# Optimization experiments

Measured on AMD Instinct MI355X. Metric: run time of the kernel, lower is better.

## Reference

```python
import jax, jax.numpy as jnp
import numpy as np

T, H, I, E, TOP_K = 4096, 2048, 1024, 16, 2
I_SHARED = 1024  # moe_intermediate_size * n_shared_experts


def _silu_and_mul(gu):
    g, u = jnp.split(gu, 2, axis=-1)
    return jax.nn.silu(g) * u


def setup_inputs() -> dict:
    key = jax.random.key(0)
    ks = jax.random.split(key, 8)
    s = 0.02
    return {
        "hidden_states": jax.random.normal(ks[0], (T, H), jnp.float32),
        "gate_w": jax.random.normal(ks[1], (E, H), jnp.float32) * s,          # router
        "w1": jax.random.normal(ks[2], (E, 2 * I, H), jnp.float32) * s,       # expert gate_up
        "b1": jax.random.normal(ks[3], (E, 2 * I), jnp.float32) * s,
        "w2": jax.random.normal(ks[4], (E, H, I), jnp.float32) * s,           # expert down
        "sg_w": jax.random.normal(ks[5], (2 * I_SHARED, H), jnp.float32) * s, # shared gate_up
        "sg_b": jax.random.normal(ks[6], (2 * I_SHARED,), jnp.float32) * s,
        "sd_w": jax.random.normal(ks[7], (H, I_SHARED), jnp.float32) * s,     # shared down
    }


def reference(hidden_states, gate_w, w1, b1, w2, sg_w, sg_b, sd_w):
    x = hidden_states  # [T, H]

    # shared expert MLP (gate_up has bias, down does not)
    shared = _silu_and_mul(x @ sg_w.T + sg_b) @ sd_w.T  # [T, H]

    # router: softmax -> top-k -> renormalize (norm_topk_prob=True)
    probs = jax.nn.softmax(x @ gate_w.T, axis=-1)       # [T, E]
    wts, idx = jax.lax.top_k(probs, TOP_K)              # [T, k]
    wts = wts / jnp.sum(wts, axis=-1, keepdims=True)

    # per-expert combine coefficient: coef[e, t] = sum_k wts[t,k] * (idx[t,k]==e)
    coef = jnp.sum(jax.nn.one_hot(idx, E, dtype=x.dtype) * wts[..., None], axis=1).T  # [E, T]

    def body(acc, params):
        w1e, b1e, w2e, ce = params
        a = _silu_and_mul(x @ w1e.T + b1e)   # [T, I]
        return acc + ce[:, None] * (a @ w2e.T), None

    out, _ = jax.lax.scan(body, jnp.zeros_like(x), (w1, b1, w2, coef))
    return out + shared
```

## Files before the change

kernel.cpp:

```cpp
#include <hip/hip_runtime.h>
#include <hip/hip_bf16.h>
#include <stdint.h>

#define T_TOK 4096
#define H_DIM 2048
#define I_DIM 1024
#define NEXP  16
#define NROWS 16384

typedef short bf16x8 __attribute__((ext_vector_type(8)));
typedef float f32x4  __attribute__((ext_vector_type(4)));
typedef unsigned short u16;
typedef unsigned short u16x8 __attribute__((ext_vector_type(8)));

__device__ __forceinline__ u16 f2b(float f) {
  union { __hip_bfloat16 h; u16 u; } cv;
  cv.h = __float2bfloat16(f);
  return cv.u;
}

__device__ __forceinline__ void gload16(const void* g, void* l) {
  __builtin_amdgcn_global_load_lds((const __attribute__((address_space(1))) void*)g,
                                   (__attribute__((address_space(3))) void*)l, 16, 0, 0);
}

__device__ __forceinline__ void cvt_seg8(const float4* __restrict__ s, u16x8* __restrict__ d,
                                         int N8, int gid, int stride) {
  for (int i = gid; i < N8; i += stride) {
    float4 v0 = s[2 * i];
    float4 v1 = s[2 * i + 1];
    u16x8 o;
    o[0] = f2b(v0.x); o[1] = f2b(v0.y); o[2] = f2b(v0.z); o[3] = f2b(v0.w);
    o[4] = f2b(v1.x); o[5] = f2b(v1.y); o[6] = f2b(v1.z); o[7] = f2b(v1.w);
    __builtin_nontemporal_store(o, &d[i]);
  }
}

__global__ __launch_bounds__(256) void cvtall_kernel(
    const float4* __restrict__ w1, const float4* __restrict__ sgw,
    const float4* __restrict__ w2, const float4* __restrict__ sdw,
    u16x8* __restrict__ W1cat, u16x8* __restrict__ W2cat) {
  const int N0 = 16 * 2048 * 2048 / 8;
  const int N1 = 2048 * 2048 / 8;
  const int N2 = 16 * 2048 * 1024 / 8;
  const int N3 = 2048 * 1024 / 8;
  int gid = blockIdx.x * 256 + threadIdx.x;
  int stride = gridDim.x * 256;
  cvt_seg8(w1,  W1cat,      N0, gid, stride);
  cvt_seg8(sgw, W1cat + N0, N1, gid, stride);
  cvt_seg8(w2,  W2cat,      N2, gid, stride);
  cvt_seg8(sdw, W2cat + N2, N3, gid, stride);
}

__global__ __launch_bounds__(256) void router_kernel(const float* __restrict__ x,
                                                     const float* __restrict__ gw,
                                                     int* __restrict__ sel,
                                                     float* __restrict__ selw,
                                                     int* __restrict__ counts,
                                                     u16* __restrict__ x_bf) {
  int t = blockIdx.x;
  int tid = threadIdx.x;
  const float* xr = x + (size_t)t * H_DIM;
  double p[NEXP];
#pragma unroll
  for (int e = 0; e < NEXP; ++e) p[e] = 0.0;
  bf16x8 xs;
#pragma unroll
  for (int j = 0; j < 8; ++j) {
    int h = tid * 8 + j;
    float xf = xr[h];
    xs[j] = (short)f2b(xf);
    double xv = (double)xf;
#pragma unroll
    for (int e = 0; e < NEXP; ++e) p[e] += xv * (double)gw[e * H_DIM + h];
  }
  *(bf16x8*)(x_bf + (size_t)t * H_DIM + tid * 8) = xs;
#pragma unroll
  for (int e = 0; e < NEXP; ++e) {
#pragma unroll
    for (int off = 32; off > 0; off >>= 1) p[e] += __shfl_down(p[e], off);
  }
  __shared__ double sm[4][NEXP];
  int w = tid >> 6;
  if ((tid & 63) == 0) {
#pragma unroll
    for (int e = 0; e < NEXP; ++e) sm[w][e] = p[e];
  }
  __syncthreads();
  if (tid == 0) {
    double l0 = -1e300, l1 = -1e300;
    int e0 = 0, e1 = 0;
    for (int e = 0; e < NEXP; ++e) {
      double v = sm[0][e] + sm[1][e] + sm[2][e] + sm[3][e];
      if (v > l0) { l1 = l0; e1 = e0; l0 = v; e0 = e; }
      else if (v > l1) { l1 = v; e1 = e; }
    }
    double w0 = 1.0 / (1.0 + exp(l1 - l0));
    sel[t * 2 + 0] = e0;
    sel[t * 2 + 1] = e1;
    selw[t * 2 + 0] = (float)w0;
    selw[t * 2 + 1] = (float)(1.0 - w0);
    atomicAdd(&counts[e0], 1);
    atomicAdd(&counts[e1], 1);
  }
}

__global__ void prefix_kernel(const int* __restrict__ counts, int* __restrict__ rowbase) {
  if (threadIdx.x == 0 && blockIdx.x == 0) {
    int acc = 0;
    for (int e = 0; e < NEXP; ++e) {
      rowbase[e] = acc;
      acc += (counts[e] + 127) & ~127;
    }
    rowbase[NEXP] = acc;
  }
}

__global__ __launch_bounds__(256) void scatter_kernel(const int* __restrict__ sel,
                                                      const float* __restrict__ selw,
                                                      const int* __restrict__ rowbase,
                                                      int* __restrict__ cursor,
                                                      int* __restrict__ tok_of_row,
                                                      float* __restrict__ coef_of_row) {
  int idx = blockIdx.x * 256 + threadIdx.x;
  if (idx < T_TOK * 2) {
    int t = idx >> 1;
    int e = sel[idx];
    int slot = atomicAdd(&cursor[e], 1);
    int row = rowbase[e] + slot;
    tok_of_row[row] = t;
    coef_of_row[row] = selw[idx];
  } else if (idx < T_TOK * 3) {
    int t = idx - T_TOK * 2;
    int sb = rowbase[NEXP];
    tok_of_row[sb + t] = t;
    coef_of_row[sb + t] = 1.0f;
  }
}


__global__ __launch_bounds__(256, 4) void gemm1_kernel(
    const u16* __restrict__ x_bf, const u16* __restrict__ W1cat,
    const float* __restrict__ b1, const float* __restrict__ sg_b,
    const int* __restrict__ tok_of_row, const int* __restrict__ counts,
    const int* __restrict__ rowbase, u16* __restrict__ abuf) {
  int nt = blockIdx.x, rt = blockIdx.y, e = blockIdx.z;
  int n_e = (e < NEXP) ? counts[e] : T_TOK;
  if (rt * 128 >= n_e) return;
  int rbase = rowbase[e];
  int n_valid = n_e - rt * 128;
  if (n_valid > 128) n_valid = 128;

  __shared__ short As[128 * 64];
  __shared__ short Bs[128 * 64];
  __shared__ int Ts[128];

  int tid = threadIdx.x;
  if (tid < 128)
    Ts[tid] = (rt * 128 + tid < n_e) ? tok_of_row[rbase + rt * 128 + tid] : 0;
  __syncthreads();

  int wavebase = tid & 0xC0;
  const u16* srcA[4];
  short* dstA[4];
  const u16* srcB[4];
  short* dstB[4];
#pragma unroll
  for (int p = 0; p < 4; ++p) {
    int c = p * 256 + tid;
    int r = c >> 3;
    int koff = ((c & 7) * 8) ^ ((r & 7) << 3);
    int tok = Ts[r];
    srcA[p] = x_bf + (size_t)tok * H_DIM + koff;
    dstA[p] = &As[(p * 256 + wavebase) * 8];
    int gr = (r < 64) ? (nt * 64 + r) : (I_DIM + nt * 64 + (r - 64));
    srcB[p] = W1cat + ((size_t)e * (2 * I_DIM) + gr) * H_DIM + koff;
    dstB[p] = &Bs[(p * 256 + wavebase) * 8];
  }

  f32x4 acc[4][4];
#pragma unroll
  for (int m = 0; m < 4; ++m)
#pragma unroll
    for (int n = 0; n < 4; ++n) acc[m][n] = (f32x4){0.f, 0.f, 0.f, 0.f};

  int lane = tid & 63, w = tid >> 6, wr = w >> 1, wc = w & 1;
  int laneq = lane & 15, hi = lane >> 4;

  for (int kt = 0; kt < H_DIM / 64; ++kt) {
    if (kt) __syncthreads();
#pragma unroll
    for (int p = 0; p < 4; ++p) gload16(srcA[p] + kt * 64, dstA[p]);
#pragma unroll
    for (int p = 0; p < 4; ++p) gload16(srcB[p] + kt * 64, dstB[p]);
    __syncthreads();
#pragma unroll
    for (int ks = 0; ks < 2; ++ks) {
      bf16x8 a[4], b[4];
#pragma unroll
      for (int f = 0; f < 4; ++f) {
        int rowA = wr * 64 + f * 16 + laneq;
        a[f] = *(const bf16x8*)(As + rowA * 64 + ((ks * 32 + hi * 8) ^ ((rowA & 7) << 3)));
        int rowB = ((f < 2) ? (wc * 32 + f * 16) : (64 + wc * 32 + (f - 2) * 16)) + laneq;
        b[f] = *(const bf16x8*)(Bs + rowB * 64 + ((ks * 32 + hi * 8) ^ ((rowB & 7) << 3)));
      }
#pragma unroll
      for (int f = 0; f < 4; ++f)
#pragma unroll
        for (int fn = 0; fn < 4; ++fn)
          acc[f][fn] = __builtin_amdgcn_mfma_f32_16x16x32_bf16(a[f], b[fn], acc[f][fn], 0, 0, 0);
    }
  }

  const float* bias = (e < NEXP) ? (b1 + (size_t)e * (2 * I_DIM)) : sg_b;
#pragma unroll
  for (int nf = 0; nf < 2; ++nf) {
    int j = nt * 64 + wc * 32 + nf * 16 + laneq;
    float bg = bias[j];
    float bu = bias[I_DIM + j];
#pragma unroll
    for (int mf = 0; mf < 4; ++mf) {
#pragma unroll
      for (int reg = 0; reg < 4; ++reg) {
        int r = wr * 64 + mf * 16 + hi * 4 + reg;
        if (r < n_valid) {
          float g = acc[mf][nf][reg] + bg;
          float u = acc[mf][nf + 2][reg] + bu;
          float s = g / (1.0f + __expf(-g));
          abuf[(size_t)(rbase + rt * 128 + r) * I_DIM + j] = f2b(s * u);
        }
      }
    }
  }
}

template <int ATOMIC>
__global__ __launch_bounds__(256, 4) void gemm2_kernel(
    const u16* __restrict__ abuf, const u16* __restrict__ W2cat,
    const int* __restrict__ tok_of_row, const float* __restrict__ coef_of_row,
    const int* __restrict__ counts, const int* __restrict__ rowbase,
    float* __restrict__ out, int e_force) {
  int nt = blockIdx.x, rt = blockIdx.y;
  int e = (e_force >= 0) ? e_force : (int)blockIdx.z;
  int n_e = (e < NEXP) ? counts[e] : T_TOK;
  if (rt * 128 >= n_e) return;
  int rbase = rowbase[e];
  int n_valid = n_e - rt * 128;
  if (n_valid > 128) n_valid = 128;

  __shared__ short As[128 * 64];
  __shared__ short Bs[128 * 64];
  __shared__ int Ts[128];
  __shared__ float Cs[128];

  int tid = threadIdx.x;
  if (tid < 128) {
    bool valid = rt * 128 + tid < n_e;
    int row = rbase + rt * 128 + tid;
    Ts[tid] = valid ? tok_of_row[row] : 0;
    Cs[tid] = valid ? coef_of_row[row] : 0.0f;
  }
  __syncthreads();

  int wavebase = tid & 0xC0;
  const u16* srcA[4];
  short* dstA[4];
  const u16* srcB[4];
  short* dstB[4];
#pragma unroll
  for (int p = 0; p < 4; ++p) {
    int c = p * 256 + tid;
    int r = c >> 3;
    int koff = ((c & 7) * 8) ^ ((r & 7) << 3);
    srcA[p] = abuf + (size_t)(rbase + rt * 128 + r) * I_DIM + koff;
    dstA[p] = &As[(p * 256 + wavebase) * 8];
    srcB[p] = W2cat + ((size_t)e * H_DIM + nt * 128 + r) * I_DIM + koff;
    dstB[p] = &Bs[(p * 256 + wavebase) * 8];
  }

  f32x4 acc[4][4];
#pragma unroll
  for (int m = 0; m < 4; ++m)
#pragma unroll
    for (int n = 0; n < 4; ++n) acc[m][n] = (f32x4){0.f, 0.f, 0.f, 0.f};

  int lane = tid & 63, w = tid >> 6, wr = w >> 1, wc = w & 1;
  int laneq = lane & 15, hi = lane >> 4;

  for (int kt = 0; kt < I_DIM / 64; ++kt) {
    if (kt) __syncthreads();
#pragma unroll
    for (int p = 0; p < 4; ++p) gload16(srcA[p] + kt * 64, dstA[p]);
#pragma unroll
    for (int p = 0; p < 4; ++p) gload16(srcB[p] + kt * 64, dstB[p]);
    __syncthreads();
#pragma unroll
    for (int ks = 0; ks < 2; ++ks) {
      bf16x8 a[4], b[4];
#pragma unroll
      for (int f = 0; f < 4; ++f) {
        int rowA = wr * 64 + f * 16 + laneq;
        int rowB = wc * 64 + f * 16 + laneq;
        a[f] = *(const bf16x8*)(As + rowA * 64 + ((ks * 32 + hi * 8) ^ ((rowA & 7) << 3)));
        b[f] = *(const bf16x8*)(Bs + rowB * 64 + ((ks * 32 + hi * 8) ^ ((rowB & 7) << 3)));
      }
#pragma unroll
      for (int f = 0; f < 4; ++f)
#pragma unroll
        for (int fn = 0; fn < 4; ++fn)
          acc[f][fn] = __builtin_amdgcn_mfma_f32_16x16x32_bf16(a[f], b[fn], acc[f][fn], 0, 0, 0);
    }
  }

#pragma unroll
  for (int mf = 0; mf < 4; ++mf) {
#pragma unroll
    for (int nf = 0; nf < 4; ++nf) {
      int col = nt * 128 + wc * 64 + nf * 16 + laneq;
#pragma unroll
      for (int reg = 0; reg < 4; ++reg) {
        int r = wr * 64 + mf * 16 + hi * 4 + reg;
        if (r < n_valid) {
          int tok = Ts[r];
          float val = acc[mf][nf][reg] * Cs[r];
          float* p = out + (size_t)tok * H_DIM + col;
          if (ATOMIC) atomicAdd(p, val);
          else *p = val;
        }
      }
    }
  }
}

extern "C" void kernel_launch(void* const* d_in, const int* in_sizes, int n_in,
                              void* d_out, int out_size, void* d_ws, size_t ws_size,
                              hipStream_t stream) {
  const float* x    = (const float*)d_in[0];
  const float* gate_w = (const float*)d_in[1];
  const float* w1   = (const float*)d_in[2];
  const float* b1   = (const float*)d_in[3];
  const float* w2   = (const float*)d_in[4];
  const float* sg_w = (const float*)d_in[5];
  const float* sg_b = (const float*)d_in[6];
  const float* sd_w = (const float*)d_in[7];
  float* out = (float*)d_out;

  uint8_t* ws = (uint8_t*)d_ws;
  size_t off = 0;
  auto alloc = [&](size_t bytes) -> void* {
    void* p = ws + off;
    off += (bytes + 255) & ~(size_t)255;
    return p;
  };
  u16*  W1cat = (u16*)alloc((size_t)17 * 2048 * 2048 * 2);
  u16*  W2cat = (u16*)alloc((size_t)17 * 2048 * 1024 * 2);
  u16*  x_bf  = (u16*)alloc((size_t)T_TOK * H_DIM * 2);
  u16*  abuf  = (u16*)alloc((size_t)NROWS * I_DIM * 2);
  int*  tok_of_row  = (int*)alloc((size_t)NROWS * 4);
  float* coef_of_row = (float*)alloc((size_t)NROWS * 4);
  int*  sel   = (int*)alloc((size_t)T_TOK * 2 * 4);
  float* selw = (float*)alloc((size_t)T_TOK * 2 * 4);
  int*  counts  = (int*)alloc(256);
  int*  cursor  = (int*)alloc(256);
  int*  rowbase = (int*)alloc(256);
  (void)ws_size; (void)in_sizes; (void)n_in; (void)out_size;

  hipMemsetAsync(counts, 0, 512, stream);

  cvtall_kernel<<<dim3(4096), dim3(256), 0, stream>>>(
      (const float4*)w1, (const float4*)sg_w, (const float4*)w2, (const float4*)sd_w,
      (u16x8*)W1cat, (u16x8*)W2cat);

  router_kernel<<<dim3(T_TOK), dim3(256), 0, stream>>>(x, gate_w, sel, selw, counts, x_bf);
  prefix_kernel<<<dim3(1), dim3(64), 0, stream>>>(counts, rowbase);
  scatter_kernel<<<dim3(48), dim3(256), 0, stream>>>(sel, selw, rowbase, cursor, tok_of_row, coef_of_row);

  gemm1_kernel<<<dim3(16, 32, 17), dim3(256), 0, stream>>>(
      x_bf, W1cat, b1, sg_b, tok_of_row, counts, rowbase, abuf);

  gemm2_kernel<0><<<dim3(16, 32, 1), dim3(256), 0, stream>>>(
      abuf, W2cat, tok_of_row, coef_of_row, counts, rowbase, out, NEXP);
  gemm2_kernel<1><<<dim3(16, 32, 16), dim3(256), 0, stream>>>(
      abuf, W2cat, tok_of_row, coef_of_row, counts, rowbase, out, -1);
}
```

Measured before the change: 527.7 us.

## Fuse fp32-to-bf16 weight conversion into GEMM tile loads

Drops the standalone pass that converts all expert and shared weights to bf16 in a workspace. Both GEMM kernels now stage fp32 weight tiles into LDS with a swizzled layout and convert to bf16 when forming MFMA operands. This removes a large read-write pass over the weights, but doubles B-tile LDS size and global bytes per tile, adds conversion ALU work in the inner loop, and lowers the occupancy target to 3 blocks.

New measurement: 474.1 us. 10.2% less time.

```diff
diff --git a/kernel.cpp b/kernel.cpp
--- a/kernel.cpp
+++ b/kernel.cpp
@@ -11,7 +11,6 @@
 typedef short bf16x8 __attribute__((ext_vector_type(8)));
 typedef float f32x4  __attribute__((ext_vector_type(4)));
 typedef unsigned short u16;
-typedef unsigned short u16x8 __attribute__((ext_vector_type(8)));
 
 __device__ __forceinline__ u16 f2b(float f) {
   union { __hip_bfloat16 h; u16 u; } cv;
@@ -24,32 +23,15 @@
                                    (__attribute__((address_space(3))) void*)l, 16, 0, 0);
 }
 
-__device__ __forceinline__ void cvt_seg8(const float4* __restrict__ s, u16x8* __restrict__ d,
-                                         int N8, int gid, int stride) {
-  for (int i = gid; i < N8; i += stride) {
-    float4 v0 = s[2 * i];
-    float4 v1 = s[2 * i + 1];
-    u16x8 o;
-    o[0] = f2b(v0.x); o[1] = f2b(v0.y); o[2] = f2b(v0.z); o[3] = f2b(v0.w);
-    o[4] = f2b(v1.x); o[5] = f2b(v1.y); o[6] = f2b(v1.z); o[7] = f2b(v1.w);
-    __builtin_nontemporal_store(o, &d[i]);
-  }
-}
-
-__global__ __launch_bounds__(256) void cvtall_kernel(
-    const float4* __restrict__ w1, const float4* __restrict__ sgw,
-    const float4* __restrict__ w2, const float4* __restrict__ sdw,
-    u16x8* __restrict__ W1cat, u16x8* __restrict__ W2cat) {
-  const int N0 = 16 * 2048 * 2048 / 8;
-  const int N1 = 2048 * 2048 / 8;
-  const int N2 = 16 * 2048 * 1024 / 8;
-  const int N3 = 2048 * 1024 / 8;
-  int gid = blockIdx.x * 256 + threadIdx.x;
-  int stride = gridDim.x * 256;
-  cvt_seg8(w1,  W1cat,      N0, gid, stride);
-  cvt_seg8(sgw, W1cat + N0, N1, gid, stride);
-  cvt_seg8(w2,  W2cat,      N2, gid, stride);
-  cvt_seg8(sdw, W2cat + N2, N3, gid, stride);
+__device__ __forceinline__ bf16x8 cvt_frag(const float* p) {
+  f32x4 v0 = *(const f32x4*)p;
+  f32x4 v1 = *(const f32x4*)(p + 4);
+  bf16x8 o;
+  o[0] = (short)f2b(v0[0]); o[1] = (short)f2b(v0[1]);
+  o[2] = (short)f2b(v0[2]); o[3] = (short)f2b(v0[3]);
+  o[4] = (short)f2b(v1[0]); o[5] = (short)f2b(v1[1]);
+  o[6] = (short)f2b(v1[2]); o[7] = (short)f2b(v1[3]);
+  return o;
 }
 
 __global__ __launch_bounds__(256) void router_kernel(const float* __restrict__ x,
@@ -139,8 +121,9 @@
 }
 
 
-__global__ __launch_bounds__(256, 4) void gemm1_kernel(
-    const u16* __restrict__ x_bf, const u16* __restrict__ W1cat,
+__global__ __launch_bounds__(256, 3) void gemm1_kernel(
+    const u16* __restrict__ x_bf, const float* __restrict__ w1,
+    const float* __restrict__ sg_w,
     const float* __restrict__ b1, const float* __restrict__ sg_b,
     const int* __restrict__ tok_of_row, const int* __restrict__ counts,
     const int* __restrict__ rowbase, u16* __restrict__ abuf) {
@@ -152,7 +135,7 @@
   if (n_valid > 128) n_valid = 128;
 
   __shared__ short As[128 * 64];
-  __shared__ short Bs[128 * 64];
+  __shared__ float Bsf[128 * 64];
   __shared__ int Ts[128];
 
   int tid = threadIdx.x;
@@ -163,8 +146,6 @@
   int wavebase = tid & 0xC0;
   const u16* srcA[4];
   short* dstA[4];
-  const u16* srcB[4];
-  short* dstB[4];
 #pragma unroll
   for (int p = 0; p < 4; ++p) {
     int c = p * 256 + tid;
@@ -173,9 +154,18 @@
     int tok = Ts[r];
     srcA[p] = x_bf + (size_t)tok * H_DIM + koff;
     dstA[p] = &As[(p * 256 + wavebase) * 8];
+  }
+  const float* Wexp = (e < NEXP) ? (w1 + (size_t)e * (2 * I_DIM) * H_DIM) : sg_w;
+  const float* srcB[8];
+  float* dstB[8];
+#pragma unroll
+  for (int p = 0; p < 8; ++p) {
+    int c = p * 256 + tid;
+    int r = c >> 4;
+    int eoff = ((c & 15) ^ (2 * (r & 7))) * 4;
     int gr = (r < 64) ? (nt * 64 + r) : (I_DIM + nt * 64 + (r - 64));
-    srcB[p] = W1cat + ((size_t)e * (2 * I_DIM) + gr) * H_DIM + koff;
-    dstB[p] = &Bs[(p * 256 + wavebase) * 8];
+    srcB[p] = Wexp + (size_t)gr * H_DIM + eoff;
+    dstB[p] = &Bsf[(p * 256 + wavebase) * 4];
   }
 
   f32x4 acc[4][4];
@@ -192,7 +182,7 @@
 #pragma unroll
     for (int p = 0; p < 4; ++p) gload16(srcA[p] + kt * 64, dstA[p]);
 #pragma unroll
-    for (int p = 0; p < 4; ++p) gload16(srcB[p] + kt * 64, dstB[p]);
+    for (int p = 0; p < 8; ++p) gload16(srcB[p] + kt * 64, dstB[p]);
     __syncthreads();
 #pragma unroll
     for (int ks = 0; ks < 2; ++ks) {
@@ -202,7 +192,8 @@
         int rowA = wr * 64 + f * 16 + laneq;
         a[f] = *(const bf16x8*)(As + rowA * 64 + ((ks * 32 + hi * 8) ^ ((rowA & 7) << 3)));
         int rowB = ((f < 2) ? (wc * 32 + f * 16) : (64 + wc * 32 + (f - 2) * 16)) + laneq;
-        b[f] = *(const bf16x8*)(Bs + rowB * 64 + ((ks * 32 + hi * 8) ^ ((rowB & 7) << 3)));
+        int cc = (ks * 8 + hi * 2) ^ (2 * (rowB & 7));
+        b[f] = cvt_frag(Bsf + rowB * 64 + cc * 4);
       }
 #pragma unroll
       for (int f = 0; f < 4; ++f)
@@ -235,8 +226,9 @@
 }
 
 template <int ATOMIC>
-__global__ __launch_bounds__(256, 4) void gemm2_kernel(
-    const u16* __restrict__ abuf, const u16* __restrict__ W2cat,
+__global__ __launch_bounds__(256, 3) void gemm2_kernel(
+    const u16* __restrict__ abuf, const float* __restrict__ w2,
+    const float* __restrict__ sd_w,
     const int* __restrict__ tok_of_row, const float* __restrict__ coef_of_row,
     const int* __restrict__ counts, const int* __restrict__ rowbase,
     float* __restrict__ out, int e_force) {
@@ -249,7 +241,7 @@
   if (n_valid > 128) n_valid = 128;
 
   __shared__ short As[128 * 64];
-  __shared__ short Bs[128 * 64];
+  __shared__ float Bsf[128 * 64];
   __shared__ int Ts[128];
   __shared__ float Cs[128];
 
@@ -265,8 +257,6 @@
   int wavebase = tid & 0xC0;
   const u16* srcA[4];
   short* dstA[4];
-  const u16* srcB[4];
-  short* dstB[4];
 #pragma unroll
   for (int p = 0; p < 4; ++p) {
     int c = p * 256 + tid;
@@ -274,8 +264,17 @@
     int koff = ((c & 7) * 8) ^ ((r & 7) << 3);
     srcA[p] = abuf + (size_t)(rbase + rt * 128 + r) * I_DIM + koff;
     dstA[p] = &As[(p * 256 + wavebase) * 8];
-    srcB[p] = W2cat + ((size_t)e * H_DIM + nt * 128 + r) * I_DIM + koff;
-    dstB[p] = &Bs[(p * 256 + wavebase) * 8];
+  }
+  const float* Wexp = (e < NEXP) ? (w2 + (size_t)e * H_DIM * I_DIM) : sd_w;
+  const float* srcB[8];
+  float* dstB[8];
+#pragma unroll
+  for (int p = 0; p < 8; ++p) {
+    int c = p * 256 + tid;
+    int r = c >> 4;
+    int eoff = ((c & 15) ^ (2 * (r & 7))) * 4;
+    srcB[p] = Wexp + (size_t)(nt * 128 + r) * I_DIM + eoff;
+    dstB[p] = &Bsf[(p * 256 + wavebase) * 4];
   }
 
   f32x4 acc[4][4];
@@ -292,7 +291,7 @@
 #pragma unroll
     for (int p = 0; p < 4; ++p) gload16(srcA[p] + kt * 64, dstA[p]);
 #pragma unroll
-    for (int p = 0; p < 4; ++p) gload16(srcB[p] + kt * 64, dstB[p]);
+    for (int p = 0; p < 8; ++p) gload16(srcB[p] + kt * 64, dstB[p]);
     __syncthreads();
 #pragma unroll
     for (int ks = 0; ks < 2; ++ks) {
@@ -302,7 +301,8 @@
         int rowA = wr * 64 + f * 16 + laneq;
         int rowB = wc * 64 + f * 16 + laneq;
         a[f] = *(const bf16x8*)(As + rowA * 64 + ((ks * 32 + hi * 8) ^ ((rowA & 7) << 3)));
-        b[f] = *(const bf16x8*)(Bs + rowB * 64 + ((ks * 32 + hi * 8) ^ ((rowB & 7) << 3)));
+        int cc = (ks * 8 + hi * 2) ^ (2 * (rowB & 7));
+        b[f] = cvt_frag(Bsf + rowB * 64 + cc * 4);
       }
 #pragma unroll
       for (int f = 0; f < 4; ++f)
@@ -352,8 +352,6 @@
     off += (bytes + 255) & ~(size_t)255;
     return p;
   };
-  u16*  W1cat = (u16*)alloc((size_t)17 * 2048 * 2048 * 2);
-  u16*  W2cat = (u16*)alloc((size_t)17 * 2048 * 1024 * 2);
   u16*  x_bf  = (u16*)alloc((size_t)T_TOK * H_DIM * 2);
   u16*  abuf  = (u16*)alloc((size_t)NROWS * I_DIM * 2);
   int*  tok_of_row  = (int*)alloc((size_t)NROWS * 4);
@@ -367,19 +365,15 @@
 
   hipMemsetAsync(counts, 0, 512, stream);
 
-  cvtall_kernel<<<dim3(4096), dim3(256), 0, stream>>>(
-      (const float4*)w1, (const float4*)sg_w, (const float4*)w2, (const float4*)sd_w,
-      (u16x8*)W1cat, (u16x8*)W2cat);
-
   router_kernel<<<dim3(T_TOK), dim3(256), 0, stream>>>(x, gate_w, sel, selw, counts, x_bf);
   prefix_kernel<<<dim3(1), dim3(64), 0, stream>>>(counts, rowbase);
   scatter_kernel<<<dim3(48), dim3(256), 0, stream>>>(sel, selw, rowbase, cursor, tok_of_row, coef_of_row);
 
   gemm1_kernel<<<dim3(16, 32, 17), dim3(256), 0, stream>>>(
-      x_bf, W1cat, b1, sg_b, tok_of_row, counts, rowbase, abuf);
+      x_bf, w1, sg_w, b1, sg_b, tok_of_row, counts, rowbase, abuf);
 
   gemm2_kernel<0><<<dim3(16, 32, 1), dim3(256), 0, stream>>>(
-      abuf, W2cat, tok_of_row, coef_of_row, counts, rowbase, out, NEXP);
+      abuf, w2, sd_w, tok_of_row, coef_of_row, counts, rowbase, out, NEXP);
   gemm2_kernel<1><<<dim3(16, 32, 16), dim3(256), 0, stream>>>(
-      abuf, W2cat, tok_of_row, coef_of_row, counts, rowbase, out, -1);
-}
+      abuf, w2, sd_w, tok_of_row, coef_of_row, counts, rowbase, out, -1);
+}
```
